# Optimization experiments

Measured on AMD Instinct MI355X. Metric: run time of the kernel, lower is better.

## Reference

```python
import jax, jax.numpy as jnp
import numpy as np

N_EMBD = 768
N_HEAD = 12


def setup_inputs() -> dict:
    key = jax.random.key(0)
    ks = jax.random.split(key, 5)
    B, T, C = 8, 1024, N_EMBD
    s_in = 1.0 / np.sqrt(C)
    x = jax.random.normal(ks[0], (B, T, C), dtype=jnp.float32)
    w_attn = jax.random.normal(ks[1], (C, 3 * C), dtype=jnp.float32) * s_in
    b_attn = jnp.zeros((3 * C,), dtype=jnp.float32)
    w_proj = jax.random.normal(ks[2], (C, C), dtype=jnp.float32) * s_in
    b_proj = jnp.zeros((C,), dtype=jnp.float32)
    return {"x": x, "w_attn": w_attn, "b_attn": b_attn,
            "w_proj": w_proj, "b_proj": b_proj}


def reference(x, w_attn, b_attn, w_proj, b_proj):
    B, T, C = x.shape
    H, hs = N_HEAD, C // N_HEAD
    qkv = x @ w_attn + b_attn                      # [B,T,3C]
    q, k, v = jnp.split(qkv, 3, axis=-1)
    # [B,H,T,hs]
    q = q.reshape(B, T, H, hs).transpose(0, 2, 1, 3)
    k = k.reshape(B, T, H, hs).transpose(0, 2, 1, 3)
    v = v.reshape(B, T, H, hs).transpose(0, 2, 1, 3)
    att = jnp.einsum('bhqd,bhkd->bhqk', q, k) * (1.0 / np.sqrt(hs))
    causal = jnp.tril(jnp.ones((T, T), dtype=bool))
    att = jnp.where(causal, att, -jnp.inf)
    att = jax.nn.softmax(att, axis=-1)
    y = jnp.einsum('bhqk,bhkd->bhqd', att, v)      # [B,H,T,hs]
    y = y.transpose(0, 2, 1, 3).reshape(B, T, C)
    return y @ w_proj + b_proj
```

## Files before the change

kernel.cpp:

```cpp
#include <hip/hip_runtime.h>
#include <hip/hip_bf16.h>
#include <stdint.h>

typedef unsigned short u16;
typedef short short8 __attribute__((ext_vector_type(8)));
typedef short short4v __attribute__((ext_vector_type(4)));
typedef float floatx4 __attribute__((ext_vector_type(4)));

__device__ __forceinline__ float b2f(u16 v) {
  union { unsigned int u; float f; } c; c.u = ((unsigned int)v) << 16; return c.f;
}
__device__ __forceinline__ u16 f2b(float f) {
  union { float f; unsigned int u; } c; c.f = f;
  unsigned int u = c.u;
  return (u16)((u + 0x7fffu + ((u >> 16) & 1u)) >> 16);
}

__device__ __forceinline__ void gld_lds16(const u16* g, u16* l) {
  __builtin_amdgcn_global_load_lds(
      (const __attribute__((address_space(1))) unsigned int*)g,
      (__attribute__((address_space(3))) unsigned int*)l,
      16, 0, 0);
}

__device__ __forceinline__ void tile_transpose_f2b(
    const float* __restrict__ in, u16* __restrict__ out,
    int inRS, int outRS, int rb, int cb, int tid)
{
  __shared__ __align__(16) u16 t[64][72];
  const int r = tid >> 2, sg = tid & 3;
  const float* ip = in + (long)(rb + r) * inRS + cb + sg * 16;
#pragma unroll
  for (int i = 0; i < 16; i += 4) {
    float4 f = *(const float4*)(ip + i);
    t[r][sg * 16 + i]     = f2b(f.x);
    t[r][sg * 16 + i + 1] = f2b(f.y);
    t[r][sg * 16 + i + 2] = f2b(f.z);
    t[r][sg * 16 + i + 3] = f2b(f.w);
  }
  __syncthreads();
  short8 v0, v1;
#pragma unroll
  for (int i = 0; i < 8; i++) v0[i] = (short)t[sg * 16 + i][r];
#pragma unroll
  for (int i = 0; i < 8; i++) v1[i] = (short)t[sg * 16 + 8 + i][r];
  *(short8*)(out + (long)(cb + r) * outRS + rb + sg * 16)     = v0;
  *(short8*)(out + (long)(cb + r) * outRS + rb + sg * 16 + 8) = v1;
}

__global__ __launch_bounds__(256) void prep(
    const float* __restrict__ x, u16* __restrict__ xb,
    const float* __restrict__ w_attn, u16* __restrict__ wTa,
    const float* __restrict__ w_proj, u16* __restrict__ wTp)
{
  const int bid = blockIdx.x, tid = threadIdx.x;
  if (bid < 6144) {
    int i = (bid * 256 + tid) * 4;
    float4 f = *(const float4*)(x + i);
    short4v v;
    v[0] = (short)f2b(f.x); v[1] = (short)f2b(f.y);
    v[2] = (short)f2b(f.z); v[3] = (short)f2b(f.w);
    *(short4v*)(xb + i) = v;
  } else if (bid < 6576) {
    int t = bid - 6144;
    tile_transpose_f2b(w_attn, wTa, 2304, 768, (t / 36) * 64, (t % 36) * 64, tid);
  } else {
    int t = bid - 6576;
    tile_transpose_f2b(w_proj, wTp, 768, 768, (t / 12) * 64, (t % 12) * 64, tid);
  }
}

__device__ __forceinline__ void store_out(u16* p, float v)  { *p = f2b(v); }
__device__ __forceinline__ void store_out(float* p, float v) { *p = v; }

template <int BM>
__device__ __forceinline__ void stage(
    const u16* __restrict__ A, const u16* __restrict__ Bt,
    long rowbase, long colbase, int K, int k0,
    u16* dA, u16* dB, int tid)
{
  const int c0 = tid, c1 = tid + 256;
  const int ar0 = c0 >> 2, ak0 = (c0 & 3) * 8;
  const int ar1 = c1 >> 2, ak1 = (c1 & 3) * 8;
  gld_lds16(A + (rowbase + ar0) * K + k0 + ak0, dA + c0 * 8);
  if (BM == 128)
    gld_lds16(A + (rowbase + ar1) * K + k0 + ak1, dA + c1 * 8);
  gld_lds16(Bt + (colbase + ar0) * K + k0 + ak0, dB + c0 * 8);
  gld_lds16(Bt + (colbase + ar1) * K + k0 + ak1, dB + c1 * 8);
}

template <typename OT, int BM, bool SPLIT>
__global__ __launch_bounds__(256) void gemm_bt_bias(
    const u16* __restrict__ A, const u16* __restrict__ Bt,
    const float* __restrict__ bias, OT* __restrict__ C, u16* __restrict__ vT,
    int M, int N, int K, int strideC)
{
  constexpr int WNF = (BM == 128) ? 4 : 2;
  __shared__ __align__(16) u16 sA[2][BM * 32];
  __shared__ __align__(16) u16 sB[2][128 * 32];
  const int tid = threadIdx.x;
  const int lane = tid & 63;
  const int wave = tid >> 6;
  const int wm = (BM == 128) ? (wave >> 1) * 64 : 0;
  const int wn = (BM == 128) ? (wave & 1) * 64 : wave * 32;
  const int l15 = lane & 15;
  const int q = lane >> 4;
  const long rowbase = (long)blockIdx.y * BM;
  const long colbase = (long)blockIdx.x * 128;

  floatx4 acc[4][WNF];
#pragma unroll
  for (int i = 0; i < 4; i++)
#pragma unroll
    for (int j = 0; j < WNF; j++) acc[i][j] = (floatx4){0.f, 0.f, 0.f, 0.f};

  stage<BM>(A, Bt, rowbase, colbase, K, 0, sA[0], sB[0], tid);
  __syncthreads();

  const int NIT = K / 32;
  for (int it = 0; it < NIT; ++it) {
    const int cur = it & 1;
    if (it + 1 < NIT)
      stage<BM>(A, Bt, rowbase, colbase, K, (it + 1) * 32, sA[cur ^ 1], sB[cur ^ 1], tid);
    short8 af[4], bf[WNF];
#pragma unroll
    for (int mt = 0; mt < 4; mt++)
      af[mt] = *(const short8*)(sA[cur] + (wm + mt * 16 + l15) * 32 + q * 8);
#pragma unroll
    for (int nt = 0; nt < WNF; nt++)
      bf[nt] = *(const short8*)(sB[cur] + (wn + nt * 16 + l15) * 32 + q * 8);
#pragma unroll
    for (int mt = 0; mt < 4; mt++)
#pragma unroll
      for (int nt = 0; nt < WNF; nt++)
        acc[mt][nt] = __builtin_amdgcn_mfma_f32_16x16x32_bf16(af[mt], bf[nt], acc[mt][nt], 0, 0, 0);
    if (it + 1 < NIT) __syncthreads();
  }

  if (SPLIT && colbase >= 1536) {
    const long b = rowbase >> 10;
    const int t0b = (int)(rowbase & 1023) + wm;
#pragma unroll
    for (int nt = 0; nt < WNF; nt++) {
      const int col = (int)colbase + wn + nt * 16 + l15;
      const float bv = bias[col];
      const int dloc = col - 1536;
      u16* bp = vT + (b * 12 + (dloc >> 6)) * 65536L + (long)(dloc & 63) * 1024;
#pragma unroll
      for (int mt = 0; mt < 4; mt++) {
        short4v pv;
#pragma unroll
        for (int r = 0; r < 4; r++) pv[r] = (short)f2b(acc[mt][nt][r] + bv);
        *(short4v*)(bp + t0b + mt * 16 + q * 4) = pv;
      }
    }
  } else {
#pragma unroll
    for (int nt = 0; nt < WNF; nt++) {
      const long col = colbase + wn + nt * 16 + l15;
      const float bv = bias[col];
#pragma unroll
      for (int mt = 0; mt < 4; mt++)
#pragma unroll
        for (int r = 0; r < 4; r++) {
          const long row = rowbase + wm + mt * 16 + q * 4 + r;
          store_out(C + row * strideC + col, acc[mt][nt][r] + bv);
        }
    }
  }
}

#define QKV_K 768
#define QKV_NT 24

__global__ __launch_bounds__(512, 2) void gemm_qkv_8ph(
    const u16* __restrict__ A, const u16* __restrict__ Bt,
    const float* __restrict__ bias, u16* __restrict__ qkOut, u16* __restrict__ vT)
{
  __shared__ __align__(16) u16 sA[4][256 * 32];
  __shared__ __align__(16) u16 sB[4][288 * 32];

  const int tid = threadIdx.x;
  const int lane = tid & 63;
  const int l15 = lane & 15, q = lane >> 4;
  const int wave = tid >> 6;
  const int wm = (wave >> 1) * 64;
  const int wn = (wave & 1) * 144;
  const long rowbase = (long)blockIdx.y * 256;
  const long colbase = (long)blockIdx.x * 288;
  const int xq = ((q ^ ((l15 >> 1) & 3)) << 3);

  const int ca0 = tid, ca1 = tid + 512;
  const u16* pa0 = A + (rowbase + (ca0 >> 2)) * QKV_K + ((((ca0 & 3) ^ ((ca0 >> 3) & 3))) << 3);
  const u16* pa1 = A + (rowbase + (ca1 >> 2)) * QKV_K + ((((ca1 & 3) ^ ((ca1 >> 3) & 3))) << 3);
  const int cb0 = tid, cb1 = tid + 512, cb2 = tid + 1024;
  const u16* pb0 = Bt + (colbase + (cb0 >> 2)) * QKV_K + ((((cb0 & 3) ^ ((cb0 >> 3) & 3))) << 3);
  const u16* pb1 = Bt + (colbase + (cb1 >> 2)) * QKV_K + ((((cb1 & 3) ^ ((cb1 >> 3) & 3))) << 3);
  const u16* pb2 = Bt + (colbase + (cb2 >> 2) - (tid < 128 ? 0 : 224)) * QKV_K
                      + ((((cb2 & 3) ^ ((cb2 >> 3) & 3))) << 3);
  const bool b3 = (tid < 128);

#define STAGE_A(t, s) do { \
    const long k0_ = (long)(t) * 32; \
    gld_lds16(pa0 + k0_, &sA[s][ca0 * 8]); \
    gld_lds16(pa1 + k0_, &sA[s][ca1 * 8]); } while (0)
#define STAGE_B(t, s) do { \
    const long k0_ = (long)(t) * 32; \
    gld_lds16(pb0 + k0_, &sB[s][cb0 * 8]); \
    gld_lds16(pb1 + k0_, &sB[s][cb1 * 8]); \
    if (b3) gld_lds16(pb2 + k0_, &sB[s][cb2 * 8]); } while (0)

  floatx4 acc[4][9];
#pragma unroll
  for (int i = 0; i < 4; i++)
#pragma unroll
    for (int n = 0; n < 9; n++) acc[i][n] = (floatx4){0.f, 0.f, 0.f, 0.f};

  STAGE_A(0, 0); STAGE_B(0, 0);
  STAGE_A(1, 1); STAGE_B(1, 1);
  STAGE_A(2, 2); STAGE_B(2, 2);
  asm volatile("s_waitcnt vmcnt(8)" ::: "memory");
  __builtin_amdgcn_s_barrier();

#pragma unroll 4
  for (int j = 0; j < QKV_NT; ++j) {
    const int slot = j & 3;
    const u16* ap = sA[slot];
    const u16* bp = sB[slot];

    short8 bf[9];
#pragma unroll
    for (int nt = 0; nt < 9; nt++)
      bf[nt] = *(const short8*)(bp + (wn + nt * 16 + l15) * 32 + xq);
    short8 a0 = *(const short8*)(ap + (wm + l15) * 32 + xq);
    short8 a1 = *(const short8*)(ap + (wm + 16 + l15) * 32 + xq);
    if (j + 3 < QKV_NT) STAGE_A(j + 3, (j + 3) & 3);
    __builtin_amdgcn_s_setprio(1);
#pragma unroll
    for (int nt = 0; nt < 9; nt++)
      acc[0][nt] = __builtin_amdgcn_mfma_f32_16x16x32_bf16(a0, bf[nt], acc[0][nt], 0, 0, 0);
#pragma unroll
    for (int nt = 0; nt < 9; nt++)
      acc[1][nt] = __builtin_amdgcn_mfma_f32_16x16x32_bf16(a1, bf[nt], acc[1][nt], 0, 0, 0);
    __builtin_amdgcn_s_setprio(0);

    short8 a2 = *(const short8*)(ap + (wm + 32 + l15) * 32 + xq);
    short8 a3 = *(const short8*)(ap + (wm + 48 + l15) * 32 + xq);
    if (j + 3 < QKV_NT) STAGE_B(j + 3, (j + 3) & 3);
    __builtin_amdgcn_s_setprio(1);
#pragma unroll
    for (int nt = 0; nt < 9; nt++)
      acc[2][nt] = __builtin_amdgcn_mfma_f32_16x16x32_bf16(a2, bf[nt], acc[2][nt], 0, 0, 0);
#pragma unroll
    for (int nt = 0; nt < 9; nt++)
      acc[3][nt] = __builtin_amdgcn_mfma_f32_16x16x32_bf16(a3, bf[nt], acc[3][nt], 0, 0, 0);
    __builtin_amdgcn_s_setprio(0);

    if (j < QKV_NT - 1) {
      if (j + 3 < QKV_NT)      asm volatile("s_waitcnt vmcnt(8)" ::: "memory");
      else if (j + 2 < QKV_NT) asm volatile("s_waitcnt vmcnt(4)" ::: "memory");
      else                     asm volatile("s_waitcnt vmcnt(0)" ::: "memory");
      __builtin_amdgcn_s_barrier();
    }
  }
#undef STAGE_A
#undef STAGE_B

#pragma unroll
  for (int nt = 0; nt < 9; nt++) {
    const int fragc = (int)colbase + wn + nt * 16;
    const int col = fragc + l15;
    const float bv = bias[col];
    if (fragc >= 1536) {
      const long bb = rowbase >> 10;
      const int dloc = col - 1536;
      u16* op = vT + (bb * 12 + (dloc >> 6)) * 65536L + (long)(dloc & 63) * 1024;
      const int t0 = (int)(rowbase & 1023) + wm;
#pragma unroll
      for (int mt = 0; mt < 4; mt++) {
        short4v pv;
#pragma unroll
        for (int r = 0; r < 4; r++) pv[r] = (short)f2b(acc[mt][nt][r] + bv);
        *(short4v*)(op + t0 + mt * 16 + q * 4) = pv;
      }
    } else {
#pragma unroll
      for (int mt = 0; mt < 4; mt++)
#pragma unroll
        for (int r = 0; r < 4; r++) {
          const long row = rowbase + wm + mt * 16 + q * 4 + r;
          qkOut[row * 1536 + col] = f2b(acc[mt][nt][r] + bv);
        }
    }
  }
}

__global__ __launch_bounds__(256) void attn_fwd(
    const u16* __restrict__ qk, const u16* __restrict__ vT, u16* __restrict__ y)
{
  const int bh = blockIdx.x;
  const int qt = 15 - blockIdx.y;
  const int b = bh / 12, h = bh % 12;
  const long rowOff = (long)b * 1024;
  const int qb = qt * 64;

  __shared__ __align__(16) u16 sK[64 * 72];
  __shared__ __align__(16) u16 sV[2][64 * 72];
  __shared__ __align__(16) u16 sP[64 * 72];

  const int tid = threadIdx.x;
  const int lane = tid & 63, wave = tid >> 6;
  const int l15 = lane & 15, q = lane >> 4;
  const int qrow_g = qb + wave * 16 + l15;

  short8 qf[2];
  {
    const u16* qp = qk + (long)(rowOff + qrow_g) * 1536 + h * 64 + q * 8;
    short8 a0 = *(const short8*)(qp);
    short8 a1 = *(const short8*)(qp + 32);
#pragma unroll
    for (int i = 0; i < 8; i++) {
      a0[i] = (short)f2b(b2f((u16)a0[i]) * 0.125f);
      a1[i] = (short)f2b(b2f((u16)a1[i]) * 0.125f);
    }
    qf[0] = a0; qf[1] = a1;
  }

  float m_i = -1e30f, l_i = 0.f;
  floatx4 o[4];
#pragma unroll
  for (int nt = 0; nt < 4; nt++) o[nt] = (floatx4){0.f, 0.f, 0.f, 0.f};

  for (int j = 0; j <= qt; j++) {
    const int jb = j * 64;
    u16* sVc = sV[j & 1];
#pragma unroll
    for (int rep = 0; rep < 2; rep++) {
      int idx = tid + rep * 256;
      int r = idx >> 3, ch = (idx & 7) * 8;
      *(short8*)(sK + r * 72 + ch) =
          *(const short8*)(qk + (long)(rowOff + jb + r) * 1536 + 768 + h * 64 + ch);
      *(short8*)(sVc + r * 72 + ch) =
          *(const short8*)(vT + (long)bh * 65536 + (long)r * 1024 + jb + ch);
    }
    __syncthreads();

    floatx4 sf[4];
#pragma unroll
    for (int mt = 0; mt < 4; mt++) sf[mt] = (floatx4){0.f, 0.f, 0.f, 0.f};
#pragma unroll
    for (int kk = 0; kk < 2; kk++) {
#pragma unroll
      for (int mt = 0; mt < 4; mt++) {
        short8 kf = *(const short8*)(sK + (mt * 16 + l15) * 72 + kk * 32 + q * 8);
        sf[mt] = __builtin_amdgcn_mfma_f32_16x16x32_bf16(kf, qf[kk], sf[mt], 0, 0, 0);
      }
    }

    float mx = m_i;
#pragma unroll
    for (int mt = 0; mt < 4; mt++)
#pragma unroll
      for (int r = 0; r < 4; r++) {
        int key_g = jb + mt * 16 + q * 4 + r;
        float v = sf[mt][r];
        if (key_g > qrow_g) v = -1e30f;
        sf[mt][r] = v;
        mx = fmaxf(mx, v);
      }
    mx = fmaxf(mx, __shfl_xor(mx, 16));
    mx = fmaxf(mx, __shfl_xor(mx, 32));
    float al = __expf(m_i - mx);
    m_i = mx;
    float rsum = 0.f;
#pragma unroll
    for (int mt = 0; mt < 4; mt++) {
      short4v pv;
#pragma unroll
      for (int r = 0; r < 4; r++) {
        float p = __expf(sf[mt][r] - mx);
        rsum += p;
        pv[r] = (short)f2b(p);
      }
      *(short4v*)(sP + (wave * 16 + l15) * 72 + mt * 16 + q * 4) = pv;
    }
    rsum += __shfl_xor(rsum, 16);
    rsum += __shfl_xor(rsum, 32);
    l_i = l_i * al + rsum;
    __syncthreads();

    float al_r[4];
#pragma unroll
    for (int r = 0; r < 4; r++) al_r[r] = __shfl(al, q * 4 + r);
#pragma unroll
    for (int nt = 0; nt < 4; nt++)
#pragma unroll
      for (int r = 0; r < 4; r++) o[nt][r] *= al_r[r];
#pragma unroll
    for (int kk = 0; kk < 2; kk++) {
      short8 pf = *(const short8*)(sP + (wave * 16 + l15) * 72 + kk * 32 + q * 8);
#pragma unroll
      for (int nt = 0; nt < 4; nt++) {
        short8 vf = *(const short8*)(sVc + (nt * 16 + l15) * 72 + kk * 32 + q * 8);
        o[nt] = __builtin_amdgcn_mfma_f32_16x16x32_bf16(pf, vf, o[nt], 0, 0, 0);
      }
    }
  }

  float linv = 1.f / l_i;
  float li_r[4];
#pragma unroll
  for (int r = 0; r < 4; r++) li_r[r] = __shfl(linv, q * 4 + r);
#pragma unroll
  for (int nt = 0; nt < 4; nt++)
#pragma unroll
    for (int r = 0; r < 4; r++) {
      int row = qb + wave * 16 + q * 4 + r;
      int col = h * 64 + nt * 16 + l15;
      y[(rowOff + row) * 768 + col] = f2b(o[nt][r] * li_r[r]);
    }
}

extern "C" void kernel_launch(void* const* d_in, const int* in_sizes, int n_in,
                              void* d_out, int out_size, void* d_ws, size_t ws_size,
                              hipStream_t stream) {
  const float* x      = (const float*)d_in[0];
  const float* w_attn = (const float*)d_in[1];
  const float* b_attn = (const float*)d_in[2];
  const float* w_proj = (const float*)d_in[3];
  const float* b_proj = (const float*)d_in[4];
  float* out = (float*)d_out;

  char* ws = (char*)d_ws;
  u16* xb   = (u16*)ws; ws += (size_t)8192 * 768 * 2;
  u16* wTa  = (u16*)ws; ws += (size_t)2304 * 768 * 2;
  u16* wTp  = (u16*)ws; ws += (size_t)768 * 768 * 2;
  u16* qk   = (u16*)ws; ws += (size_t)8192 * 1536 * 2;
  u16* vT   = (u16*)ws; ws += (size_t)96 * 64 * 1024 * 2;
  u16* yatt = (u16*)ws; ws += (size_t)8192 * 768 * 2;

  prep<<<dim3(6720), 256, 0, stream>>>(x, xb, w_attn, wTa, w_proj, wTp);

  gemm_qkv_8ph<<<dim3(8, 32), 512, 0, stream>>>(xb, wTa, b_attn, qk, vT);

  attn_fwd<<<dim3(96, 16), 256, 0, stream>>>(qk, vT, yatt);

  gemm_bt_bias<float, 64, false><<<dim3(6, 128), 256, 0, stream>>>(
      yatt, wTp, b_proj, out, (u16*)nullptr, 8192, 768, 768, 768);
}
```

Measured before the change: 215.9 us.

## Retile QKV GEMM to 256x256 blocks with XCD-aware swizzle, enlarge proj tile

The QKV GEMM changes from 256x288 tiles on an 8x32 grid to square 256x256 tiles on a 1D grid of 288 blocks. Each wave now covers a 128x64 sub-tile, and block ids are remapped so that neighbouring tiles land on the same XCD. An extra barrier is added inside the main loop, and the output projection GEMM moves from a 64-row to a 128-row tile template. The goals are a more uniform B staging path without the partial third load, better L2 locality, and fewer projection blocks, at the cost of the added barrier and a different wave occupancy balance.

Result: faster. 207.9 us (-3.7%).

```diff
diff --git a/kernel.cpp b/kernel.cpp
--- a/kernel.cpp
+++ b/kernel.cpp
@@ -173,48 +173,46 @@
 #define QKV_K 768
 #define QKV_NT 24
 
-__global__ __launch_bounds__(512, 2) void gemm_qkv_8ph(
+__global__ __launch_bounds__(512, 2) void gemm_qkv_256(
     const u16* __restrict__ A, const u16* __restrict__ Bt,
     const float* __restrict__ bias, u16* __restrict__ qkOut, u16* __restrict__ vT)
 {
   __shared__ __align__(16) u16 sA[4][256 * 32];
-  __shared__ __align__(16) u16 sB[4][288 * 32];
+  __shared__ __align__(16) u16 sB[4][256 * 32];
+
+  const int bid0 = blockIdx.x;
+  const int wg = (bid0 & 7) * 36 + (bid0 >> 3);
+  const int bx = wg % 9;
+  const int by = wg / 9;
 
   const int tid = threadIdx.x;
   const int lane = tid & 63;
   const int l15 = lane & 15, q = lane >> 4;
   const int wave = tid >> 6;
-  const int wm = (wave >> 1) * 64;
-  const int wn = (wave & 1) * 144;
-  const long rowbase = (long)blockIdx.y * 256;
-  const long colbase = (long)blockIdx.x * 288;
+  const int wm = (wave >> 2) * 128;
+  const int wn = (wave & 3) * 64;
+  const long rowbase = (long)by * 256;
+  const long colbase = (long)bx * 256;
   const int xq = ((q ^ ((l15 >> 1) & 3)) << 3);
 
   const int ca0 = tid, ca1 = tid + 512;
   const u16* pa0 = A + (rowbase + (ca0 >> 2)) * QKV_K + ((((ca0 & 3) ^ ((ca0 >> 3) & 3))) << 3);
   const u16* pa1 = A + (rowbase + (ca1 >> 2)) * QKV_K + ((((ca1 & 3) ^ ((ca1 >> 3) & 3))) << 3);
-  const int cb0 = tid, cb1 = tid + 512, cb2 = tid + 1024;
-  const u16* pb0 = Bt + (colbase + (cb0 >> 2)) * QKV_K + ((((cb0 & 3) ^ ((cb0 >> 3) & 3))) << 3);
-  const u16* pb1 = Bt + (colbase + (cb1 >> 2)) * QKV_K + ((((cb1 & 3) ^ ((cb1 >> 3) & 3))) << 3);
-  const u16* pb2 = Bt + (colbase + (cb2 >> 2) - (tid < 128 ? 0 : 224)) * QKV_K
-                      + ((((cb2 & 3) ^ ((cb2 >> 3) & 3))) << 3);
-  const bool b3 = (tid < 128);
+  const u16* pb0 = Bt + (colbase + (ca0 >> 2)) * QKV_K + ((((ca0 & 3) ^ ((ca0 >> 3) & 3))) << 3);
+  const u16* pb1 = Bt + (colbase + (ca1 >> 2)) * QKV_K + ((((ca1 & 3) ^ ((ca1 >> 3) & 3))) << 3);
 
 #define STAGE_A(t, s) do { \
-    const long k0_ = (long)(t) * 32; \
-    gld_lds16(pa0 + k0_, &sA[s][ca0 * 8]); \
-    gld_lds16(pa1 + k0_, &sA[s][ca1 * 8]); } while (0)
+    gld_lds16(pa0 + (long)(t) * 32, &sA[s][ca0 * 8]); \
+    gld_lds16(pa1 + (long)(t) * 32, &sA[s][ca1 * 8]); } while (0)
 #define STAGE_B(t, s) do { \
-    const long k0_ = (long)(t) * 32; \
-    gld_lds16(pb0 + k0_, &sB[s][cb0 * 8]); \
-    gld_lds16(pb1 + k0_, &sB[s][cb1 * 8]); \
-    if (b3) gld_lds16(pb2 + k0_, &sB[s][cb2 * 8]); } while (0)
-
-  floatx4 acc[4][9];
-#pragma unroll
-  for (int i = 0; i < 4; i++)
-#pragma unroll
-    for (int n = 0; n < 9; n++) acc[i][n] = (floatx4){0.f, 0.f, 0.f, 0.f};
+    gld_lds16(pb0 + (long)(t) * 32, &sB[s][ca0 * 8]); \
+    gld_lds16(pb1 + (long)(t) * 32, &sB[s][ca1 * 8]); } while (0)
+
+  floatx4 acc[8][4];
+#pragma unroll
+  for (int i = 0; i < 8; i++)
+#pragma unroll
+    for (int n = 0; n < 4; n++) acc[i][n] = (floatx4){0.f, 0.f, 0.f, 0.f};
 
   STAGE_A(0, 0); STAGE_B(0, 0);
   STAGE_A(1, 1); STAGE_B(1, 1);
@@ -228,32 +226,34 @@
     const u16* ap = sA[slot];
     const u16* bp = sB[slot];
 
-    short8 bf[9];
-#pragma unroll
-    for (int nt = 0; nt < 9; nt++)
+    short8 bf[4];
+#pragma unroll
+    for (int nt = 0; nt < 4; nt++)
       bf[nt] = *(const short8*)(bp + (wn + nt * 16 + l15) * 32 + xq);
-    short8 a0 = *(const short8*)(ap + (wm + l15) * 32 + xq);
-    short8 a1 = *(const short8*)(ap + (wm + 16 + l15) * 32 + xq);
+    short8 af[4];
+#pragma unroll
+    for (int mt = 0; mt < 4; mt++)
+      af[mt] = *(const short8*)(ap + (wm + mt * 16 + l15) * 32 + xq);
     if (j + 3 < QKV_NT) STAGE_A(j + 3, (j + 3) & 3);
+    __builtin_amdgcn_s_barrier();
     __builtin_amdgcn_s_setprio(1);
 #pragma unroll
-    for (int nt = 0; nt < 9; nt++)
-      acc[0][nt] = __builtin_amdgcn_mfma_f32_16x16x32_bf16(a0, bf[nt], acc[0][nt], 0, 0, 0);
-#pragma unroll
-    for (int nt = 0; nt < 9; nt++)
-      acc[1][nt] = __builtin_amdgcn_mfma_f32_16x16x32_bf16(a1, bf[nt], acc[1][nt], 0, 0, 0);
+    for (int mt = 0; mt < 4; mt++)
+#pragma unroll
+      for (int nt = 0; nt < 4; nt++)
+        acc[mt][nt] = __builtin_amdgcn_mfma_f32_16x16x32_bf16(af[mt], bf[nt], acc[mt][nt], 0, 0, 0);
     __builtin_amdgcn_s_setprio(0);
 
-    short8 a2 = *(const short8*)(ap + (wm + 32 + l15) * 32 + xq);
-    short8 a3 = *(const short8*)(ap + (wm + 48 + l15) * 32 + xq);
+#pragma unroll
+    for (int mt = 0; mt < 4; mt++)
+      af[mt] = *(const short8*)(ap + (wm + 64 + mt * 16 + l15) * 32 + xq);
     if (j + 3 < QKV_NT) STAGE_B(j + 3, (j + 3) & 3);
     __builtin_amdgcn_s_setprio(1);
 #pragma unroll
-    for (int nt = 0; nt < 9; nt++)
-      acc[2][nt] = __builtin_amdgcn_mfma_f32_16x16x32_bf16(a2, bf[nt], acc[2][nt], 0, 0, 0);
-#pragma unroll
-    for (int nt = 0; nt < 9; nt++)
-      acc[3][nt] = __builtin_amdgcn_mfma_f32_16x16x32_bf16(a3, bf[nt], acc[3][nt], 0, 0, 0);
+    for (int mt = 0; mt < 4; mt++)
+#pragma unroll
+      for (int nt = 0; nt < 4; nt++)
+        acc[4 + mt][nt] = __builtin_amdgcn_mfma_f32_16x16x32_bf16(af[mt], bf[nt], acc[4 + mt][nt], 0, 0, 0);
     __builtin_amdgcn_s_setprio(0);
 
     if (j < QKV_NT - 1) {
@@ -266,26 +266,30 @@
 #undef STAGE_A
 #undef STAGE_B
 
-#pragma unroll
-  for (int nt = 0; nt < 9; nt++) {
-    const int fragc = (int)colbase + wn + nt * 16;
-    const int col = fragc + l15;
-    const float bv = bias[col];
-    if (fragc >= 1536) {
-      const long bb = rowbase >> 10;
+  if (colbase >= 1536) {
+    const long bb = rowbase >> 10;
+    const int t0 = (int)(rowbase & 1023) + wm;
+#pragma unroll
+    for (int nt = 0; nt < 4; nt++) {
+      const int col = (int)colbase + wn + nt * 16 + l15;
+      const float bv = bias[col];
       const int dloc = col - 1536;
       u16* op = vT + (bb * 12 + (dloc >> 6)) * 65536L + (long)(dloc & 63) * 1024;
-      const int t0 = (int)(rowbase & 1023) + wm;
-#pragma unroll
-      for (int mt = 0; mt < 4; mt++) {
+#pragma unroll
+      for (int mt = 0; mt < 8; mt++) {
         short4v pv;
 #pragma unroll
         for (int r = 0; r < 4; r++) pv[r] = (short)f2b(acc[mt][nt][r] + bv);
         *(short4v*)(op + t0 + mt * 16 + q * 4) = pv;
       }
-    } else {
-#pragma unroll
-      for (int mt = 0; mt < 4; mt++)
+    }
+  } else {
+#pragma unroll
+    for (int nt = 0; nt < 4; nt++) {
+      const long col = colbase + wn + nt * 16 + l15;
+      const float bv = bias[col];
+#pragma unroll
+      for (int mt = 0; mt < 8; mt++)
 #pragma unroll
         for (int r = 0; r < 4; r++) {
           const long row = rowbase + wm + mt * 16 + q * 4 + r;
@@ -441,10 +445,10 @@
 
   prep<<<dim3(6720), 256, 0, stream>>>(x, xb, w_attn, wTa, w_proj, wTp);
 
-  gemm_qkv_8ph<<<dim3(8, 32), 512, 0, stream>>>(xb, wTa, b_attn, qk, vT);
+  gemm_qkv_256<<<dim3(288), 512, 0, stream>>>(xb, wTa, b_attn, qk, vT);
 
   attn_fwd<<<dim3(96, 16), 256, 0, stream>>>(qk, vT, yatt);
 
-  gemm_bt_bias<float, 64, false><<<dim3(6, 128), 256, 0, stream>>>(
+  gemm_bt_bias<float, 128, false><<<dim3(6, 64), 256, 0, stream>>>(
       yatt, wTp, b_proj, out, (u16*)nullptr, 8192, 768, 768, 768);
 }
```
